# Performance work log

Measured on AMD Instinct MI355X. Metric: run time of the kernel, lower is better.

Reference implementation:

```python
import jax, jax.numpy as jnp
import numpy as np

H, NH, NL, FF, W, CMAX, V, L, G = 768, 12, 6, 3072, 256, 32, 50272, 4096, 64
DH = H // NH
SCALE = 1.0 / np.sqrt(DH)

def _ln(x, s, b, eps=1e-5):
    m = jnp.mean(x, -1, keepdims=True)
    v = jnp.mean((x - m) ** 2, -1, keepdims=True)
    return (x - m) * jax.lax.rsqrt(v + eps) * s + b

def _heads(x, B, Lx):
    return x.reshape(B, Lx, NH, DH).transpose(0, 2, 1, 3)  # [B,NH,L,DH]

def _layer(x, p, am, gpos, is_glob):
    (Wq, bq, Wk, bk, Wv, bv, Wqg, bqg, Wkg, bkg, Wvg, bvg, Wo, bo,
     ln1s, ln1b, W1, b1, W2, b2, ln2s, ln2b) = p
    B, Lx, _ = x.shape
    Nb = Lx // W
    q = _heads(x @ Wq + bq, B, Lx)
    k = _heads(x @ Wk + bk, B, Lx)
    v = _heads(x @ Wv + bv, B, Lx)
    qb = q.reshape(B, NH, Nb, W, DH)
    def ctx(t):  # gather 3 adjacent key/value blocks per query block
        tb = t.reshape(B, NH, Nb, W, DH)
        tp = jnp.pad(tb, ((0, 0), (0, 0), (1, 1), (0, 0), (0, 0)))
        return jnp.stack([tp[:, :, i:i + Nb] for i in range(3)], axis=3).reshape(B, NH, Nb, 3 * W, DH)
    k_ctx, v_ctx = ctx(k), ctx(v)
    s_loc = jnp.einsum('bhnqd,bhnkd->bhnqk', qb, k_ctx) * SCALE  # [B,NH,Nb,W,3W]
    rel = jnp.arange(3 * W)[None, :] - W - jnp.arange(W)[:, None]  # [W,3W]
    band = jnp.abs(rel) <= W
    pos = jnp.arange(Nb)[:, None] * W + jnp.arange(3 * W)[None, :] - W  # abs key pos [Nb,3W]
    inb = (pos >= 0) & (pos < Lx)
    safe = jnp.clip(pos, 0, Lx - 1)
    key_ok = inb & (~is_glob[safe]) & am[:, safe]  # [B,Nb,3W]; global keys handled separately
    mask = key_ok[:, None, :, None, :] & band[None, None, None, :, :]
    s_loc = jnp.where(mask, s_loc, -1e9)
    # every token also attends to the G global tokens (global K/V projections)
    kg = _heads(x @ Wkg + bkg, B, Lx)
    vg = _heads(x @ Wvg + bvg, B, Lx)
    kgs, vgs = kg[:, :, gpos], vg[:, :, gpos]  # [B,NH,G,DH]
    s_glb = jnp.einsum('bhnqd,bhgd->bhnqg', qb, kgs) * SCALE
    attn = jax.nn.softmax(jnp.concatenate([s_loc, s_glb], -1), axis=-1)
    a_loc, a_glb = attn[..., :3 * W], attn[..., 3 * W:]
    out = jnp.einsum('bhnqk,bhnkd->bhnqd', a_loc, v_ctx) + jnp.einsum('bhnqg,bhgd->bhnqd', a_glb, vgs)
    out = out.reshape(B, NH, Lx, DH)
    # global query rows: full attention over all positions, overwrite outputs
    qg = _heads(x @ Wqg + bqg, B, Lx)[:, :, gpos]  # [B,NH,G,DH]
    s_full = jnp.einsum('bhgd,bhld->bhgl', qg, kg) * SCALE
    s_full = jnp.where(am[:, None, None, :], s_full, -1e9)
    og = jnp.einsum('bhgl,bhld->bhgd', jax.nn.softmax(s_full, -1), vg)
    out = out.at[:, :, gpos].set(og)
    out = out.transpose(0, 2, 1, 3).reshape(B, Lx, H)
    x = _ln(x + out @ Wo + bo, ln1s, ln1b)
    h = jax.nn.gelu(x @ W1 + b1, approximate=False)
    x = _ln(x + h @ W2 + b2, ln2s, ln2b)
    return x

def _forward(floats, input_ids, attention_mask, global_positions, cand_token_id):
    (emb_tok, emb_pos, lnes, lneb,
     Wq, bq, Wk, bk, Wv, bv, Wqg, bqg, Wkg, bkg, Wvg, bvg, Wo, bo,
     ln1_s, ln1_b, W1, b1, W2, b2, ln2_s, ln2_b, Wh1, bh1, Wh2, bh2) = floats
    B, Lx = input_ids.shape
    x = _ln(emb_tok[input_ids] + emb_pos[None, :Lx], lnes, lneb)
    is_glob = jnp.zeros(Lx, bool).at[global_positions].set(True)
    layers = (Wq, bq, Wk, bk, Wv, bv, Wqg, bqg, Wkg, bkg, Wvg, bvg, Wo, bo,
              ln1_s, ln1_b, W1, b1, W2, b2, ln2_s, ln2_b)
    def step(xc, p):
        return _layer(xc, p, attention_mask, global_positions, is_glob), None
    x, _ = jax.lax.scan(step, x, layers)
    # ListwiseRankingHead: gather hidden states at [CAND] marker positions
    cand_mask = input_ids == cand_token_id
    order = jnp.argsort(jnp.where(cand_mask, 0, 1).astype(jnp.int32), axis=1)  # stable
    positions = order[:, :CMAX]
    valid = jnp.take_along_axis(cand_mask, positions, axis=1)
    g = jnp.take_along_axis(x, positions[..., None], axis=1)  # [B,CMAX,H]
    h = jax.nn.gelu(g @ Wh1 + bh1, approximate=False)  # dropout is eval no-op
    logits = (h @ Wh2 + bh2).squeeze(-1)
    return logits, valid

def setup_inputs() -> dict:
    key = jax.random.key(0)
    ks = iter(jax.random.split(key, 64))
    r = lambda shape: jax.random.normal(next(ks), shape, jnp.float32) * 0.02
    B, CAND = 1, 50265
    d = {
        'emb_tok': r((V, H)), 'emb_pos': r((L, H)),
        'ln_emb_s': jnp.ones((H,), jnp.float32), 'ln_emb_b': jnp.zeros((H,), jnp.float32),
        'Wq': r((NL, H, H)), 'bq': jnp.zeros((NL, H), jnp.float32),
        'Wk': r((NL, H, H)), 'bk': jnp.zeros((NL, H), jnp.float32),
        'Wv': r((NL, H, H)), 'bv': jnp.zeros((NL, H), jnp.float32),
        'Wqg': r((NL, H, H)), 'bqg': jnp.zeros((NL, H), jnp.float32),
        'Wkg': r((NL, H, H)), 'bkg': jnp.zeros((NL, H), jnp.float32),
        'Wvg': r((NL, H, H)), 'bvg': jnp.zeros((NL, H), jnp.float32),
        'Wo': r((NL, H, H)), 'bo': jnp.zeros((NL, H), jnp.float32),
        'ln1_s': jnp.ones((NL, H), jnp.float32), 'ln1_b': jnp.zeros((NL, H), jnp.float32),
        'W1': r((NL, H, FF)), 'b1': jnp.zeros((NL, FF), jnp.float32),
        'W2': r((NL, FF, H)), 'b2': jnp.zeros((NL, H), jnp.float32),
        'ln2_s': jnp.ones((NL, H), jnp.float32), 'ln2_b': jnp.zeros((NL, H), jnp.float32),
        'Wh1': r((H, H // 2)), 'bh1': jnp.zeros((H // 2,), jnp.float32),
        'Wh2': r((H // 2, 1)), 'bh2': jnp.zeros((1,), jnp.float32),
    }
    input_ids = jax.random.randint(next(ks), (B, L), 0, CAND, dtype=jnp.int32)
    cand_pos = 256 + 128 * jnp.arange(30)  # 30 [CAND] markers
    input_ids = input_ids.at[:, cand_pos].set(CAND)
    d['input_ids'] = input_ids
    d['attention_mask'] = jnp.ones((B, L), jnp.bool_)
    d['global_positions'] = jnp.concatenate([jnp.arange(34), cand_pos]).astype(jnp.int32)  # CLS+query+markers
    d['cand_token_id'] = CAND
    return d

def reference(emb_tok, emb_pos, ln_emb_s, ln_emb_b, Wq, bq, Wk, bk, Wv, bv,
              Wqg, bqg, Wkg, bkg, Wvg, bvg, Wo, bo, ln1_s, ln1_b,
              W1, b1, W2, b2, ln2_s, ln2_b, Wh1, bh1, Wh2, bh2,
              input_ids, attention_mask, global_positions, cand_token_id):
    floats = (emb_tok, emb_pos, ln_emb_s, ln_emb_b, Wq, bq, Wk, bk, Wv, bv,
              Wqg, bqg, Wkg, bkg, Wvg, bvg, Wo, bo, ln1_s, ln1_b,
              W1, b1, W2, b2, ln2_s, ln2_b, Wh1, bh1, Wh2, bh2)
    return _forward(floats, input_ids, attention_mask, global_positions, cand_token_id)
```

## Files before the change

### kernel.cpp

```cpp
#include <hip/hip_runtime.h>
#include <hip/hip_bf16.h>
#include <math.h>

#define H 768
#define NH 12
#define DH 64
#define NL 6
#define FF 3072
#define LL 4096
#define GG 64
#define NCMAX 32

#define MATSZ (H * H)
#define OFF_QG ((size_t)5 * MATSZ)
#define OFF_O  ((size_t)6 * MATSZ)
#define OFF_W1 ((size_t)7 * MATSZ)
#define OFF_W2 (OFF_W1 + (size_t)H * FF)
#define WT_ELEMS (OFF_W2 + (size_t)FF * H)

typedef unsigned short u16;
typedef __attribute__((ext_vector_type(8))) unsigned short us8;
typedef __attribute__((ext_vector_type(4))) unsigned short us4;
typedef __attribute__((ext_vector_type(8))) __bf16 bf16x8;
typedef __attribute__((ext_vector_type(4))) float f32x4;

__device__ __forceinline__ float bf2f(u16 u) {
  unsigned v = ((unsigned)u) << 16;
  return __builtin_bit_cast(float, v);
}
__device__ __forceinline__ u16 f2bf(float f) {
  unsigned u = __builtin_bit_cast(unsigned, f);
  unsigned r = (u + 0x7fffu + ((u >> 16) & 1u)) >> 16;
  return (u16)r;
}
__device__ __forceinline__ float geluf(float a) {
  return 0.5f * a * (1.f + erff(a * 0.70710678118654752440f));
}
__device__ __forceinline__ float wredsum(float v) {
  #pragma unroll
  for (int o = 32; o; o >>= 1) v += __shfl_xor(v, o);
  return v;
}
__device__ __forceinline__ float wredmax(float v) {
  #pragma unroll
  for (int o = 32; o; o >>= 1) v = fmaxf(v, __shfl_xor(v, o));
  return v;
}
__device__ __forceinline__ void gld16(const u16* g, u16* l) {
  __builtin_amdgcn_global_load_lds(
      (const __attribute__((address_space(1))) unsigned int*)(const void*)g,
      (__attribute__((address_space(3))) unsigned int*)(void*)l, 16, 0, 0);
}
__device__ __forceinline__ void tswz(int& bx, int& by) {
  int nx = gridDim.x, ny = gridDim.y;
  int flat = blockIdx.y * nx + blockIdx.x;
  int nwg = nx * ny;
  if ((nwg & 7) == 0) {
    int c = nwg >> 3;
    flat = (flat & 7) * c + (flat >> 3);
  }
  bx = flat % nx;
  by = flat / nx;
}

__global__ __launch_bounds__(256) void embed_ln_k(
    const float* __restrict__ et, const float* __restrict__ ep, const int* __restrict__ ids,
    const float* __restrict__ sc, const float* __restrict__ bi,
    float* __restrict__ x, u16* __restrict__ xb)
{
  int r = blockIdx.x, t = threadIdx.x;
  int tok = ids[r];
  if (tok < 0) tok = 0;
  if (tok >= 50272) tok = 50271;
  __shared__ float red[4];
  float v[3];
  #pragma unroll
  for (int e = 0; e < 3; ++e) {
    int c = t + e * 256;
    v[e] = et[(size_t)tok * H + c] + ep[(size_t)r * H + c];
  }
  float s = v[0] + v[1] + v[2];
  s = wredsum(s);
  if ((t & 63) == 0) red[t >> 6] = s;
  __syncthreads();
  float mean = (red[0] + red[1] + red[2] + red[3]) * (1.f / 768.f);
  __syncthreads();
  float q = 0.f;
  #pragma unroll
  for (int e = 0; e < 3; ++e) { float d = v[e] - mean; q += d * d; }
  q = wredsum(q);
  if ((t & 63) == 0) red[t >> 6] = q;
  __syncthreads();
  float var = (red[0] + red[1] + red[2] + red[3]) * (1.f / 768.f);
  float rs = rsqrtf(var + 1e-5f);
  #pragma unroll
  for (int e = 0; e < 3; ++e) {
    int c = t + e * 256;
    float o = (v[e] - mean) * rs * sc[c] + bi[c];
    x[(size_t)r * H + c] = o;
    xb[(size_t)r * H + c] = f2bf(o);
  }
}

__global__ __launch_bounds__(256) void ln_res_k(
    float* __restrict__ x, const float* __restrict__ bias,
    const float* __restrict__ sc, const float* __restrict__ bi, u16* __restrict__ xb)
{
  int r = blockIdx.x, t = threadIdx.x;
  __shared__ float red[4];
  float v[3];
  #pragma unroll
  for (int e = 0; e < 3; ++e) {
    int c = t + e * 256;
    v[e] = x[(size_t)r * H + c] + bias[c];
  }
  float s = v[0] + v[1] + v[2];
  s = wredsum(s);
  if ((t & 63) == 0) red[t >> 6] = s;
  __syncthreads();
  float mean = (red[0] + red[1] + red[2] + red[3]) * (1.f / 768.f);
  __syncthreads();
  float q = 0.f;
  #pragma unroll
  for (int e = 0; e < 3; ++e) { float d = v[e] - mean; q += d * d; }
  q = wredsum(q);
  if ((t & 63) == 0) red[t >> 6] = q;
  __syncthreads();
  float var = (red[0] + red[1] + red[2] + red[3]) * (1.f / 768.f);
  float rs = rsqrtf(var + 1e-5f);
  #pragma unroll
  for (int e = 0; e < 3; ++e) {
    int c = t + e * 256;
    float o = (v[e] - mean) * rs * sc[c] + bi[c];
    x[(size_t)r * H + c] = o;
    xb[(size_t)r * H + c] = f2bf(o);
  }
}

__global__ __launch_bounds__(256) void conv_layer_k(
    const float* __restrict__ Wq, const float* __restrict__ Wk, const float* __restrict__ Wv,
    const float* __restrict__ Wkg, const float* __restrict__ Wvg, const float* __restrict__ Wqg,
    const float* __restrict__ Wo, const float* __restrict__ W1, const float* __restrict__ W2,
    u16* __restrict__ wt)
{
  int bid = blockIdx.x, t = threadIdx.x;
  const float* src;
  size_t ooff;
  int K, N, tile;
  if (bid < 1008) {
    int m = bid / 144;
    tile = bid % 144;
    K = H; N = H;
    ooff = (size_t)m * MATSZ;
    src = m == 0 ? Wq : m == 1 ? Wk : m == 2 ? Wv : m == 3 ? Wkg : m == 4 ? Wvg : m == 5 ? Wqg : Wo;
  } else if (bid < 1584) {
    tile = bid - 1008;
    K = H; N = FF;
    ooff = OFF_W1;
    src = W1;
  } else {
    tile = bid - 1584;
    K = FF; N = H;
    ooff = OFF_W2;
    src = W2;
  }
  int KT = K / 64;
  int kt = tile % KT, nt = tile / KT;
  __shared__ u16 sT[64 * 72];
  #pragma unroll
  for (int it = 0; it < 16; ++it) {
    int idx = t + it * 256;
    int n = idx & 63, kk = idx >> 6;
    sT[n * 72 + kk] = f2bf(src[(size_t)(kt * 64 + kk) * N + nt * 64 + n]);
  }
  __syncthreads();
  #pragma unroll
  for (int it = 0; it < 2; ++it) {
    int idx = t + it * 256;
    int n = idx >> 3, k8 = idx & 7;
    us8 val = *reinterpret_cast<const us8*>(&sT[n * 72 + k8 * 8]);
    *reinterpret_cast<us8*>(&wt[ooff + (size_t)(nt * 64 + n) * K + kt * 64 + k8 * 8]) = val;
  }
}

template<bool GLD>
__device__ __forceinline__ void gemm_loop(
    const u16* __restrict__ A, const u16* __restrict__ Bt,
    int M, int N, int K, int m0, int n0, int kb, int ke,
    u16* lsA, u16* lsB, f32x4 acc[4][4])
{
  int t = threadIdx.x;
  int w = t >> 6, lane = t & 63;
  int cl = lane & 15, kgr = lane >> 4;
  int wm = (w >> 1) * 64, wn = (w & 1) * 64;
  us8 z8 = {0, 0, 0, 0, 0, 0, 0, 0};
  for (int k0 = kb; k0 < ke; k0 += 64) {
    if (GLD) {
      int ml = lane >> 3, k8 = lane & 7;
      #pragma unroll
      for (int it = 0; it < 4; ++it) {
        int chunk = it * 4 + w;
        int m = chunk * 8 + ml;
        gld16(A + (size_t)(m0 + m) * K + k0 + ((k8 ^ (m & 7)) * 8),
              &lsA[chunk * 512 + lane * 8]);
      }
      #pragma unroll
      for (int it = 0; it < 4; ++it) {
        int chunk = it * 4 + w;
        int n = chunk * 8 + ml;
        gld16(Bt + (size_t)(n0 + n) * K + k0 + ((k8 ^ (n & 7)) * 8),
              &lsB[chunk * 512 + lane * 8]);
      }
    } else {
      #pragma unroll
      for (int it = 0; it < 4; ++it) {
        int c = t + it * 256;
        int m = c >> 3, k8 = c & 7;
        us8 val = z8;
        int gm = m0 + m;
        if (gm < M) val = *reinterpret_cast<const us8*>(A + (size_t)gm * K + k0 + k8 * 8);
        *reinterpret_cast<us8*>(&lsA[m * 64 + ((k8 ^ (m & 7)) * 8)]) = val;
      }
      #pragma unroll
      for (int it = 0; it < 4; ++it) {
        int c = t + it * 256;
        int n = c >> 3, k8 = c & 7;
        us8 val = *reinterpret_cast<const us8*>(Bt + (size_t)(n0 + n) * K + k0 + k8 * 8);
        *reinterpret_cast<us8*>(&lsB[n * 64 + ((k8 ^ (n & 7)) * 8)]) = val;
      }
    }
    __syncthreads();
    #pragma unroll
    for (int kk = 0; kk < 2; ++kk) {
      bf16x8 fa[4], fb[4];
      int k8 = kk * 4 + kgr;
      #pragma unroll
      for (int i = 0; i < 4; ++i) {
        int mr = wm + i * 16 + cl;
        fa[i] = __builtin_bit_cast(bf16x8,
            *reinterpret_cast<const us8*>(&lsA[mr * 64 + ((k8 ^ (mr & 7)) * 8)]));
        int nr = wn + i * 16 + cl;
        fb[i] = __builtin_bit_cast(bf16x8,
            *reinterpret_cast<const us8*>(&lsB[nr * 64 + ((k8 ^ (nr & 7)) * 8)]));
      }
      #pragma unroll
      for (int i = 0; i < 4; ++i)
        #pragma unroll
        for (int j = 0; j < 4; ++j)
          acc[i][j] = __builtin_amdgcn_mfma_f32_16x16x32_bf16(fa[i], fb[j], acc[i][j], 0, 0, 0);
    }
    __syncthreads();
  }
}

template<int ACT, bool GLD>
__global__ __launch_bounds__(256) void gemm_bias_k(
    const u16* __restrict__ A, const u16* __restrict__ Bt, const float* __restrict__ bias,
    u16* __restrict__ outB, int M, int N, int K)
{
  __shared__ u16 lsA[128 * 64];
  __shared__ u16 lsB[128 * 64];
  int bx, by;
  tswz(bx, by);
  int m0 = by * 128, n0 = bx * 128;
  f32x4 zero4 = {0.f, 0.f, 0.f, 0.f};
  f32x4 acc[4][4];
  #pragma unroll
  for (int i = 0; i < 4; ++i)
    #pragma unroll
    for (int j = 0; j < 4; ++j) acc[i][j] = zero4;
  gemm_loop<GLD>(A, Bt, M, N, K, m0, n0, 0, K, lsA, lsB, acc);
  int lane = threadIdx.x & 63, w = threadIdx.x >> 6;
  int cl = lane & 15, kgr = lane >> 4;
  int wm = (w >> 1) * 64, wn = (w & 1) * 64;
  #pragma unroll
  for (int j = 0; j < 4; ++j) {
    int n = n0 + wn + j * 16 + cl;
    float bv = bias[n];
    #pragma unroll
    for (int i = 0; i < 4; ++i) {
      #pragma unroll
      for (int r = 0; r < 4; ++r) {
        int m = m0 + wm + i * 16 + kgr * 4 + r;
        if (m < M) {
          float vv = acc[i][j][r] + bv;
          if (ACT == 1) vv = geluf(vv);
          outB[(size_t)m * N + n] = f2bf(vv);
        }
      }
    }
  }
}

__global__ __launch_bounds__(256) void gemm_acc_k(
    const u16* __restrict__ A, const u16* __restrict__ Bt, float* __restrict__ outF,
    int M, int N, int K)
{
  __shared__ u16 lsA[128 * 64];
  __shared__ u16 lsB[128 * 64];
  int bx, by;
  tswz(bx, by);
  int m0 = by * 128, n0 = bx * 128;
  int z = blockIdx.z, ns = gridDim.z;
  int ks = K / ns;
  f32x4 zero4 = {0.f, 0.f, 0.f, 0.f};
  f32x4 acc[4][4];
  #pragma unroll
  for (int i = 0; i < 4; ++i)
    #pragma unroll
    for (int j = 0; j < 4; ++j) acc[i][j] = zero4;
  gemm_loop<true>(A, Bt, M, N, K, m0, n0, z * ks, (z + 1) * ks, lsA, lsB, acc);
  int lane = threadIdx.x & 63, w = threadIdx.x >> 6;
  int cl = lane & 15, kgr = lane >> 4;
  int wm = (w >> 1) * 64, wn = (w & 1) * 64;
  #pragma unroll
  for (int j = 0; j < 4; ++j) {
    int n = n0 + wn + j * 16 + cl;
    #pragma unroll
    for (int i = 0; i < 4; ++i) {
      #pragma unroll
      for (int r = 0; r < 4; ++r) {
        int m = m0 + wm + i * 16 + kgr * 4 + r;
        atomicAdd(&outF[(size_t)m * N + n], acc[i][j][r]);
      }
    }
  }
}

__global__ __launch_bounds__(256) void gemm_qkv_k(
    const u16* __restrict__ A, const u16* __restrict__ wt,
    const float* c0, const float* c1, const float* c2, const float* c3, const float* c4,
    u16* o0, u16* o1, u16* o2, u16* o3, u16* o4)
{
  __shared__ u16 lsA[128 * 64];
  __shared__ u16 lsB[128 * 64];
  int z = blockIdx.z;
  const u16* Bt = wt + (size_t)z * MATSZ;
  const float* bias = z == 0 ? c0 : z == 1 ? c1 : z == 2 ? c2 : z == 3 ? c3 : c4;
  u16* outB = z == 0 ? o0 : z == 1 ? o1 : z == 2 ? o2 : z == 3 ? o3 : o4;
  int bx, by;
  tswz(bx, by);
  int m0 = by * 128, n0 = bx * 128;
  f32x4 zero4 = {0.f, 0.f, 0.f, 0.f};
  f32x4 acc[4][4];
  #pragma unroll
  for (int i = 0; i < 4; ++i)
    #pragma unroll
    for (int j = 0; j < 4; ++j) acc[i][j] = zero4;
  gemm_loop<true>(A, Bt, LL, H, H, m0, n0, 0, H, lsA, lsB, acc);
  int lane = threadIdx.x & 63, w = threadIdx.x >> 6;
  int cl = lane & 15, kgr = lane >> 4;
  int wm = (w >> 1) * 64, wn = (w & 1) * 64;
  #pragma unroll
  for (int j = 0; j < 4; ++j) {
    int n = n0 + wn + j * 16 + cl;
    float bv = bias[n];
    #pragma unroll
    for (int i = 0; i < 4; ++i) {
      #pragma unroll
      for (int r = 0; r < 4; ++r) {
        int m = m0 + wm + i * 16 + kgr * 4 + r;
        outB[(size_t)m * H + n] = f2bf(acc[i][j][r] + bv);
      }
    }
  }
}

__global__ __launch_bounds__(256) void attn_local_k(
    const u16* __restrict__ q, const u16* __restrict__ k, const u16* __restrict__ v,
    const u16* __restrict__ kgp, const u16* __restrict__ vgp,
    const int* __restrict__ gpos, const unsigned char* __restrict__ isg,
    u16* __restrict__ out)
{
  int h = blockIdx.x;
  int q0 = blockIdx.y * 64;
  int nb = q0 >> 8;
  int cs = (nb - 1) * 256;
  int cstart = (q0 >> 6) & 3;
  int t = threadIdx.x;
  int w = t >> 6, lane = t & 63;
  int cl = lane & 15, g = lane >> 4;
  __shared__ u16 sK[64 * 64];
  __shared__ u16 sVt[64 * 64];
  __shared__ u16 sP[64 * 64];
  __shared__ unsigned char sOk[64];
  us8 z8 = {0, 0, 0, 0, 0, 0, 0, 0};
  f32x4 zero4 = {0.f, 0.f, 0.f, 0.f};

  int qrow = q0 + w * 16 + cl;
  bf16x8 qa[2];
  #pragma unroll
  for (int ks = 0; ks < 2; ++ks)
    qa[ks] = __builtin_bit_cast(bf16x8, *reinterpret_cast<const us8*>(
        &q[(size_t)qrow * H + h * 64 + ks * 32 + g * 8]));

  f32x4 O[4];
  #pragma unroll
  for (int dt = 0; dt < 4; ++dt) O[dt] = zero4;
  float mrow[4], lrow[4];
  #pragma unroll
  for (int r = 0; r < 4; ++r) { mrow[r] = -1e30f; lrow[r] = 0.f; }

  for (int ci = 0; ci < 10; ++ci) {
    bool isLocal = (ci < 9);
    int kbase = cs + (cstart + ci) * 64;
    #pragma unroll
    for (int it = 0; it < 2; ++it) {
      int idx = t + it * 256;
      int key = idx >> 3, d8 = idx & 7;
      us8 val = z8;
      if (isLocal) {
        int pos = kbase + key;
        if (pos >= 0 && pos < LL)
          val = *reinterpret_cast<const us8*>(&k[(size_t)pos * H + h * 64 + d8 * 8]);
      } else {
        int pos = gpos[key];
        if (pos < 0) pos = 0;
        if (pos >= LL) pos = LL - 1;
        val = *reinterpret_cast<const us8*>(&kgp[(size_t)pos * H + h * 64 + d8 * 8]);
      }
      *reinterpret_cast<us8*>(&sK[key * 64 + ((d8 ^ (key & 7)) * 8)]) = val;
    }
    #pragma unroll
    for (int it = 0; it < 2; ++it) {
      int idx = t + it * 256;
      int key = idx >> 3, d8 = idx & 7;
      us8 val = z8;
      if (isLocal) {
        int pos = kbase + key;
        if (pos >= 0 && pos < LL)
          val = *reinterpret_cast<const us8*>(&v[(size_t)pos * H + h * 64 + d8 * 8]);
      } else {
        int pos = gpos[key];
        if (pos < 0) pos = 0;
        if (pos >= LL) pos = LL - 1;
        val = *reinterpret_cast<const us8*>(&vgp[(size_t)pos * H + h * 64 + d8 * 8]);
      }
      int k8 = key >> 3, klow = key & 7;
      int kswz = (k8 ^ d8) * 8 + klow;
      #pragma unroll
      for (int u = 0; u < 8; ++u)
        sVt[(d8 * 8 + u) * 64 + kswz] = val[u];
    }
    if (t < 64) {
      int ok = 1;
      if (isLocal) {
        int pos = kbase + t;
        ok = (pos >= 0 && pos < LL) ? (isg[pos] ? 0 : 1) : 0;
      }
      sOk[t] = (unsigned char)ok;
    }
    __syncthreads();

    f32x4 S[4];
    #pragma unroll
    for (int T = 0; T < 4; ++T) {
      S[T] = zero4;
      int key = T * 16 + cl;
      #pragma unroll
      for (int ks = 0; ks < 2; ++ks) {
        bf16x8 kf = __builtin_bit_cast(bf16x8, *reinterpret_cast<const us8*>(
            &sK[key * 64 + (((ks * 4 + g) ^ (key & 7)) * 8)]));
        S[T] = __builtin_amdgcn_mfma_f32_16x16x32_bf16(qa[ks], kf, S[T], 0, 0, 0);
      }
    }
    #pragma unroll
    for (int T = 0; T < 4; ++T) {
      int key = T * 16 + cl;
      int okk = sOk[key];
      int pos = kbase + key;
      #pragma unroll
      for (int r = 0; r < 4; ++r) {
        int qp = q0 + w * 16 + g * 4 + r;
        int d = pos - qp;
        bool ok = okk && (!isLocal || (d >= -256 && d <= 256));
        S[T][r] = ok ? S[T][r] * 0.125f : -1e9f;
      }
    }
    float cm[4];
    #pragma unroll
    for (int r = 0; r < 4; ++r) {
      cm[r] = fmaxf(fmaxf(S[0][r], S[1][r]), fmaxf(S[2][r], S[3][r]));
      cm[r] = fmaxf(cm[r], __shfl_xor(cm[r], 1));
      cm[r] = fmaxf(cm[r], __shfl_xor(cm[r], 2));
      cm[r] = fmaxf(cm[r], __shfl_xor(cm[r], 4));
      cm[r] = fmaxf(cm[r], __shfl_xor(cm[r], 8));
    }
    float sc[4];
    #pragma unroll
    for (int r = 0; r < 4; ++r) {
      float mn = fmaxf(mrow[r], cm[r]);
      sc[r] = __expf(mrow[r] - mn);
      mrow[r] = mn;
    }
    float rs[4] = {0.f, 0.f, 0.f, 0.f};
    #pragma unroll
    for (int T = 0; T < 4; ++T) {
      int key = T * 16 + cl;
      #pragma unroll
      for (int r = 0; r < 4; ++r) {
        float sv = S[T][r];
        float pv = sv > -1e8f ? __expf(sv - mrow[r]) : 0.f;
        rs[r] += pv;
        int qloc = w * 16 + g * 4 + r;
        int k8s = (key >> 3) ^ (qloc & 7);
        sP[qloc * 64 + k8s * 8 + (key & 7)] = f2bf(pv);
      }
    }
    #pragma unroll
    for (int r = 0; r < 4; ++r) {
      rs[r] += __shfl_xor(rs[r], 1);
      rs[r] += __shfl_xor(rs[r], 2);
      rs[r] += __shfl_xor(rs[r], 4);
      rs[r] += __shfl_xor(rs[r], 8);
      lrow[r] = lrow[r] * sc[r] + rs[r];
    }
    #pragma unroll
    for (int dt = 0; dt < 4; ++dt)
      #pragma unroll
      for (int r = 0; r < 4; ++r) O[dt][r] *= sc[r];
    int prow = w * 16 + cl;
    #pragma unroll
    for (int ks = 0; ks < 2; ++ks) {
      bf16x8 pf = __builtin_bit_cast(bf16x8, *reinterpret_cast<const us8*>(
          &sP[prow * 64 + (((ks * 4 + g) ^ (prow & 7)) * 8)]));
      #pragma unroll
      for (int dt = 0; dt < 4; ++dt) {
        int dim = dt * 16 + cl;
        int k8s = (ks * 4 + g) ^ ((dim >> 3) & 7);
        bf16x8 vf = __builtin_bit_cast(bf16x8, *reinterpret_cast<const us8*>(
            &sVt[dim * 64 + k8s * 8]));
        O[dt] = __builtin_amdgcn_mfma_f32_16x16x32_bf16(pf, vf, O[dt], 0, 0, 0);
      }
    }
    __syncthreads();
  }
  #pragma unroll
  for (int r = 0; r < 4; ++r) {
    float inv = 1.f / lrow[r];
    int qp = q0 + w * 16 + g * 4 + r;
    #pragma unroll
    for (int dt = 0; dt < 4; ++dt)
      out[(size_t)qp * H + h * 64 + dt * 16 + cl] = f2bf(O[dt][r] * inv);
  }
}

__global__ __launch_bounds__(256) void ag_score_k(
    const u16* __restrict__ qg, const u16* __restrict__ kg, float* __restrict__ sbuf)
{
  int h = blockIdx.x;
  int kc0 = blockIdx.y * 128;
  int t = threadIdx.x;
  int w = t >> 6, lane = t & 63;
  int cl = lane & 15, g = lane >> 4;
  __shared__ u16 sK[128 * 64];
  #pragma unroll
  for (int it = 0; it < 4; ++it) {
    int c = t + it * 256;
    int key = c >> 3, d8 = c & 7;
    us8 val = *reinterpret_cast<const us8*>(&kg[(size_t)(kc0 + key) * H + h * 64 + d8 * 8]);
    *reinterpret_cast<us8*>(&sK[key * 64 + ((d8 ^ (key & 7)) * 8)]) = val;
  }
  int qrow = w * 16 + cl;
  bf16x8 qa[2];
  #pragma unroll
  for (int ks = 0; ks < 2; ++ks)
    qa[ks] = __builtin_bit_cast(bf16x8, *reinterpret_cast<const us8*>(
        &qg[(size_t)qrow * H + h * 64 + ks * 32 + g * 8]));
  __syncthreads();
  f32x4 zero4 = {0.f, 0.f, 0.f, 0.f};
  #pragma unroll
  for (int j = 0; j < 8; ++j) {
    f32x4 S = zero4;
    int key = j * 16 + cl;
    #pragma unroll
    for (int ks = 0; ks < 2; ++ks) {
      bf16x8 kf = __builtin_bit_cast(bf16x8, *reinterpret_cast<const us8*>(
          &sK[key * 64 + (((ks * 4 + g) ^ (key & 7)) * 8)]));
      S = __builtin_amdgcn_mfma_f32_16x16x32_bf16(qa[ks], kf, S, 0, 0, 0);
    }
    #pragma unroll
    for (int r = 0; r < 4; ++r) {
      int grow = w * 16 + g * 4 + r;
      sbuf[((size_t)(h * 64 + grow)) * 4096 + kc0 + key] = S[r] * 0.125f;
    }
  }
}

__global__ __launch_bounds__(256) void ag_soft_k(float* __restrict__ sbuf)
{
  int row = blockIdx.x, t = threadIdx.x;
  float* base = sbuf + (size_t)row * 4096;
  u16* pb = (u16*)(sbuf) + (size_t)row * 8192;
  __shared__ float red[4];
  f32x4 rv[4];
  #pragma unroll
  for (int it = 0; it < 4; ++it)
    rv[it] = *reinterpret_cast<const f32x4*>(base + it * 1024 + t * 4);
  float m = -1e30f;
  #pragma unroll
  for (int it = 0; it < 4; ++it)
    #pragma unroll
    for (int u = 0; u < 4; ++u) m = fmaxf(m, rv[it][u]);
  m = wredmax(m);
  if ((t & 63) == 0) red[t >> 6] = m;
  __syncthreads();
  m = fmaxf(fmaxf(red[0], red[1]), fmaxf(red[2], red[3]));
  __syncthreads();
  float s = 0.f;
  #pragma unroll
  for (int it = 0; it < 4; ++it)
    #pragma unroll
    for (int u = 0; u < 4; ++u) {
      float e = __expf(rv[it][u] - m);
      rv[it][u] = e;
      s += e;
    }
  s = wredsum(s);
  if ((t & 63) == 0) red[t >> 6] = s;
  __syncthreads();
  float inv = 1.f / (red[0] + red[1] + red[2] + red[3]);
  #pragma unroll
  for (int it = 0; it < 4; ++it) {
    us4 o;
    #pragma unroll
    for (int u = 0; u < 4; ++u) o[u] = f2bf(rv[it][u] * inv);
    *reinterpret_cast<us4*>(pb + it * 1024 + t * 4) = o;
  }
}

__global__ __launch_bounds__(256) void ag_pv_k(
    const float* __restrict__ sbuf, const u16* __restrict__ vg, float* __restrict__ obuf)
{
  int h = blockIdx.x;
  int kb0 = blockIdx.y * 256;
  int t = threadIdx.x;
  int w = t >> 6, lane = t & 63;
  int cl = lane & 15, g = lane >> 4;
  __shared__ u16 sVt[64 * 64];
  f32x4 zero4 = {0.f, 0.f, 0.f, 0.f};
  f32x4 O[4];
  #pragma unroll
  for (int dt = 0; dt < 4; ++dt) O[dt] = zero4;
  const u16* pb = (const u16*)(sbuf);
  int prow = w * 16 + cl;
  size_t pbase = (size_t)(h * 64 + prow) * 8192;

  for (int cc = 0; cc < 4; ++cc) {
    int kc = kb0 + cc * 64;
    #pragma unroll
    for (int it = 0; it < 2; ++it) {
      int idx = t + it * 256;
      int key = idx >> 3, d8 = idx & 7;
      us8 val = *reinterpret_cast<const us8*>(&vg[(size_t)(kc + key) * H + h * 64 + d8 * 8]);
      int k8 = key >> 3, klow = key & 7;
      int kswz = (k8 ^ d8) * 8 + klow;
      #pragma unroll
      for (int u = 0; u < 8; ++u)
        sVt[(d8 * 8 + u) * 64 + kswz] = val[u];
    }
    __syncthreads();
    #pragma unroll
    for (int ks = 0; ks < 2; ++ks) {
      bf16x8 pf = __builtin_bit_cast(bf16x8, *reinterpret_cast<const us8*>(
          pb + pbase + kc + (ks * 4 + g) * 8));
      #pragma unroll
      for (int dt = 0; dt < 4; ++dt) {
        int dim = dt * 16 + cl;
        int k8s = (ks * 4 + g) ^ ((dim >> 3) & 7);
        bf16x8 vf = __builtin_bit_cast(bf16x8, *reinterpret_cast<const us8*>(
            &sVt[dim * 64 + k8s * 8]));
        O[dt] = __builtin_amdgcn_mfma_f32_16x16x32_bf16(pf, vf, O[dt], 0, 0, 0);
      }
    }
    __syncthreads();
  }
  #pragma unroll
  for (int r = 0; r < 4; ++r) {
    int grow = w * 16 + g * 4 + r;
    #pragma unroll
    for (int dt = 0; dt < 4; ++dt)
      atomicAdd(&obuf[((size_t)h * 64 + grow) * 64 + dt * 16 + cl], O[dt][r]);
  }
}

__global__ __launch_bounds__(256) void ag_write_k(
    float* __restrict__ obuf, const int* __restrict__ gpos, u16* __restrict__ out)
{
  int g = blockIdx.x, t = threadIdx.x;
  int gp = gpos[g];
  if (gp < 0) gp = 0;
  if (gp >= LL) gp = LL - 1;
  #pragma unroll
  for (int e = 0; e < 3; ++e) {
    int c = t + e * 256;
    int h = c >> 6, d = c & 63;
    size_t idx = ((size_t)h * 64 + g) * 64 + d;
    out[(size_t)gp * H + c] = f2bf(obuf[idx]);
    obuf[idx] = 0.f;
  }
}

__global__ void isglob_k(const int* __restrict__ gpos, unsigned char* __restrict__ isg) {
  int t = threadIdx.x;
  for (int i = t; i < LL; i += 256) isg[i] = 0;
  __syncthreads();
  if (t < GG) {
    int gp = gpos[t];
    if (gp >= 0 && gp < LL) isg[gp] = 1;
  }
}

__global__ void gather_k(const u16* __restrict__ xb, const int* __restrict__ gpos,
                         u16* __restrict__ xgb) {
  int g = blockIdx.x, t = threadIdx.x;
  int p = gpos[g];
  if (p < 0) p = 0;
  if (p >= LL) p = LL - 1;
  #pragma unroll
  for (int e = 0; e < 3; ++e)
    xgb[(size_t)g * H + t + e * 256] = xb[(size_t)p * H + t + e * 256];
}

__global__ void positions_k(const int* __restrict__ ids, const int* __restrict__ candp,
                            int* __restrict__ posb, float* __restrict__ outp) {
  int t = threadIdx.x;
  int cand = candp[0];
  __shared__ int cnt[257];
  int base = t * 16, c0 = 0;
  for (int u = 0; u < 16; ++u) c0 += (ids[base + u] == cand) ? 1 : 0;
  cnt[t + 1] = c0;
  __syncthreads();
  if (t == 0) {
    cnt[0] = 0;
    for (int i2 = 1; i2 <= 256; ++i2) cnt[i2] += cnt[i2 - 1];
  }
  __syncthreads();
  int ncand = cnt[256];
  int cr = cnt[t];
  for (int u = 0; u < 16; ++u) {
    int i2 = base + u;
    bool isC = (ids[i2] == cand);
    if (isC) {
      if (cr < NCMAX) posb[cr] = i2;
      cr++;
    } else {
      int nc = i2 - cr;
      int slot = ncand + nc;
      if (slot < NCMAX && nc >= 0) posb[slot] = i2;
    }
  }
  if (t < NCMAX) outp[NCMAX + t] = (t < ncand) ? 1.f : 0.f;
}

__global__ __launch_bounds__(256) void head_k(
    const float* __restrict__ x, const int* __restrict__ posb,
    const float* __restrict__ Wh1, const float* __restrict__ bh1,
    const float* __restrict__ Wh2, const float* __restrict__ bh2, float* __restrict__ outp) {
  int s = blockIdx.x, t = threadIdx.x;
  int p = posb[s];
  if (p < 0) p = 0;
  if (p >= LL) p = LL - 1;
  __shared__ float sx[H];
  __shared__ float sh[384];
  __shared__ float red[4];
  #pragma unroll
  for (int e = 0; e < 3; ++e) sx[t + e * 256] = x[(size_t)p * H + t + e * 256];
  __syncthreads();
  for (int j = t; j < 384; j += 256) {
    float a = bh1[j];
    for (int c = 0; c < H; ++c) a += sx[c] * Wh1[(size_t)c * 384 + j];
    sh[j] = geluf(a);
  }
  __syncthreads();
  float part = 0.f;
  for (int j = t; j < 384; j += 256) part += sh[j] * Wh2[j];
  part = wredsum(part);
  if ((t & 63) == 0) red[t >> 6] = part;
  __syncthreads();
  if (t == 0) {
    float tot = red[0] + red[1] + red[2] + red[3] + bh2[0];
    outp[s] = tot;
  }
}

extern "C" void kernel_launch(void* const* d_in, const int* in_sizes, int n_in,
                              void* d_out, int out_size, void* d_ws, size_t ws_size,
                              hipStream_t stream) {
  const float* emb_tok = (const float*)d_in[0];
  const float* emb_pos = (const float*)d_in[1];
  const float* lnes = (const float*)d_in[2];
  const float* lneb = (const float*)d_in[3];
  const float* Wq = (const float*)d_in[4];
  const float* bq = (const float*)d_in[5];
  const float* Wk = (const float*)d_in[6];
  const float* bk = (const float*)d_in[7];
  const float* Wv = (const float*)d_in[8];
  const float* bv = (const float*)d_in[9];
  const float* Wqg = (const float*)d_in[10];
  const float* bqg = (const float*)d_in[11];
  const float* Wkg = (const float*)d_in[12];
  const float* bkg = (const float*)d_in[13];
  const float* Wvg = (const float*)d_in[14];
  const float* bvg = (const float*)d_in[15];
  const float* Wo = (const float*)d_in[16];
  const float* bo = (const float*)d_in[17];
  const float* ln1s = (const float*)d_in[18];
  const float* ln1b = (const float*)d_in[19];
  const float* W1 = (const float*)d_in[20];
  const float* b1 = (const float*)d_in[21];
  const float* W2 = (const float*)d_in[22];
  const float* b2 = (const float*)d_in[23];
  const float* ln2s = (const float*)d_in[24];
  const float* ln2b = (const float*)d_in[25];
  const float* Wh1 = (const float*)d_in[26];
  const float* bh1 = (const float*)d_in[27];
  const float* Wh2 = (const float*)d_in[28];
  const float* bh2 = (const float*)d_in[29];
  const int* ids = (const int*)d_in[30];
  int i_gpos = 32, i_cand = 33;
  if (!(n_in >= 34 && in_sizes[32] == GG)) {
    if (n_in >= 33 && in_sizes[31] == GG) { i_gpos = 31; i_cand = 32; }
  }
  const int* gpos = (const int*)d_in[i_gpos];
  const int* cand = (const int*)d_in[i_cand];
  float* outp = (float*)d_out;

  char* p = (char*)d_ws;
  auto alloc = [&](size_t bytes) {
    char* r = p;
    p += (bytes + 255) & ~(size_t)255;
    return r;
  };
  float* x = (float*)alloc((size_t)LL * H * 4);
  u16* xb = (u16*)alloc((size_t)LL * H * 2);
  u16* qb = (u16*)alloc((size_t)LL * H * 2);
  u16* kb = (u16*)alloc((size_t)LL * H * 2);
  u16* vb = (u16*)alloc((size_t)LL * H * 2);
  u16* kgb = (u16*)alloc((size_t)LL * H * 2);
  u16* vgb = (u16*)alloc((size_t)LL * H * 2);
  u16* ob = (u16*)alloc((size_t)LL * H * 2);
  u16* qgb = (u16*)alloc((size_t)GG * H * 2);
  u16* xgb = (u16*)alloc((size_t)GG * H * 2);
  unsigned char* isg = (unsigned char*)alloc(LL);
  int* posb = (int*)alloc(64 * 4);
  u16* wtb = (u16*)alloc(WT_ELEMS * 2);
  float* sbuf = (float*)alloc((size_t)NH * 64 * 4096 * 4);
  float* obuf = (float*)alloc((size_t)NH * 64 * 64 * 4);
  u16* hb = qb;

  hipMemsetAsync(obuf, 0, (size_t)NH * 64 * 64 * 4, stream);

  embed_ln_k<<<LL, 256, 0, stream>>>(emb_tok, emb_pos, ids, lnes, lneb, x, xb);
  isglob_k<<<1, 256, 0, stream>>>(gpos, isg);
  positions_k<<<1, 256, 0, stream>>>(ids, cand, posb, outp);

  dim3 gP2(H / 128, LL / 128, 2);
  dim3 gP4(H / 128, LL / 128, 4);
  dim3 gF(FF / 128, LL / 128);
  dim3 gQKV(H / 128, LL / 128, 5);
  for (int l = 0; l < NL; ++l) {
    size_t lo = (size_t)l * H * H;
    conv_layer_k<<<2160, 256, 0, stream>>>(
        Wq + lo, Wk + lo, Wv + lo, Wkg + lo, Wvg + lo, Wqg + lo, Wo + lo,
        W1 + (size_t)l * H * FF, W2 + (size_t)l * FF * H, wtb);
    gemm_qkv_k<<<gQKV, 256, 0, stream>>>(xb, wtb,
        bq + l * H, bk + l * H, bv + l * H, bkg + l * H, bvg + l * H,
        qb, kb, vb, kgb, vgb);
    gather_k<<<GG, 256, 0, stream>>>(xb, gpos, xgb);
    gemm_bias_k<0, true><<<dim3(H / 128, 1), 256, 0, stream>>>(
        xgb, wtb + OFF_QG, bqg + l * H, qgb, GG, H, H);
    attn_local_k<<<dim3(NH, LL / 64), 256, 0, stream>>>(qb, kb, vb, kgb, vgb, gpos, isg, ob);
    ag_score_k<<<dim3(NH, LL / 128), 256, 0, stream>>>(qgb, kgb, sbuf);
    ag_soft_k<<<NH * 64, 256, 0, stream>>>(sbuf);
    ag_pv_k<<<dim3(NH, LL / 256), 256, 0, stream>>>(sbuf, vgb, obuf);
    ag_write_k<<<GG, 256, 0, stream>>>(obuf, gpos, ob);
    gemm_acc_k<<<gP2, 256, 0, stream>>>(ob, wtb + OFF_O, x, LL, H, H);
    ln_res_k<<<LL, 256, 0, stream>>>(x, bo + l * H, ln1s + l * H, ln1b + l * H, xb);
    gemm_bias_k<1, true><<<gF, 256, 0, stream>>>(
        xb, wtb + OFF_W1, b1 + l * FF, hb, LL, FF, H);
    gemm_acc_k<<<gP4, 256, 0, stream>>>(hb, wtb + OFF_W2, x, LL, H, FF);
    ln_res_k<<<LL, 256, 0, stream>>>(x, b2 + l * H, ln2s + l * H, ln2b + l * H, xb);
  }
  head_k<<<NCMAX, 256, 0, stream>>>(x, posb, Wh1, bh1, Wh2, bh2, outp);
}
```

Baseline: 1.653 ms.

## Batch weight conversion, fuse global-query GEMM into QKV, replace split-K atomics with partials

Weight conversion to bf16 now runs once for all six layers in a single launch instead of once per layer. The global-query projection becomes a sixth z-slice of the QKV GEMM, so a separate launch goes away. The split-K output and FFN GEMMs write per-slice partial buffers that the LayerNorm kernel sums, replacing fp32 atomicAdd on the residual. The attention K-tile loads switch to direct global-to-LDS loads. In exchange it uses more workspace (all layers' weights plus four full-size fp32 partial buffers) and adds extra partial-buffer reads in LayerNorm.

```diff
diff --git a/kernel.cpp b/kernel.cpp
--- a/kernel.cpp
+++ b/kernel.cpp
@@ -102,8 +102,9 @@
   }
 }
 
-__global__ __launch_bounds__(256) void ln_res_k(
-    float* __restrict__ x, const float* __restrict__ bias,
+template<int Z>
+__global__ __launch_bounds__(256) void ln_res2_k(
+    float* __restrict__ x, const float* __restrict__ part, const float* __restrict__ bias,
     const float* __restrict__ sc, const float* __restrict__ bi, u16* __restrict__ xb)
 {
   int r = blockIdx.x, t = threadIdx.x;
@@ -112,7 +113,11 @@
   #pragma unroll
   for (int e = 0; e < 3; ++e) {
     int c = t + e * 256;
-    v[e] = x[(size_t)r * H + c] + bias[c];
+    float a = x[(size_t)r * H + c] + bias[c];
+    #pragma unroll
+    for (int z = 0; z < Z; ++z)
+      a += part[(size_t)z * LL * H + (size_t)r * H + c];
+    v[e] = a;
   }
   float s = v[0] + v[1] + v[2];
   s = wredsum(s);
@@ -137,13 +142,17 @@
   }
 }
 
-__global__ __launch_bounds__(256) void conv_layer_k(
+__global__ __launch_bounds__(256) void conv_all_k(
     const float* __restrict__ Wq, const float* __restrict__ Wk, const float* __restrict__ Wv,
     const float* __restrict__ Wkg, const float* __restrict__ Wvg, const float* __restrict__ Wqg,
     const float* __restrict__ Wo, const float* __restrict__ W1, const float* __restrict__ W2,
     u16* __restrict__ wt)
 {
+  int l = blockIdx.y;
   int bid = blockIdx.x, t = threadIdx.x;
+  size_t lo = (size_t)l * MATSZ;
+  size_t lf = (size_t)l * H * FF;
+  u16* wto = wt + (size_t)l * WT_ELEMS;
   const float* src;
   size_t ooff;
   int K, N, tile;
@@ -152,17 +161,17 @@
     tile = bid % 144;
     K = H; N = H;
     ooff = (size_t)m * MATSZ;
-    src = m == 0 ? Wq : m == 1 ? Wk : m == 2 ? Wv : m == 3 ? Wkg : m == 4 ? Wvg : m == 5 ? Wqg : Wo;
+    src = (m == 0 ? Wq : m == 1 ? Wk : m == 2 ? Wv : m == 3 ? Wkg : m == 4 ? Wvg : m == 5 ? Wqg : Wo) + lo;
   } else if (bid < 1584) {
     tile = bid - 1008;
     K = H; N = FF;
     ooff = OFF_W1;
-    src = W1;
+    src = W1 + lf;
   } else {
     tile = bid - 1584;
     K = FF; N = H;
     ooff = OFF_W2;
-    src = W2;
+    src = W2 + lf;
   }
   int KT = K / 64;
   int kt = tile % KT, nt = tile / KT;
@@ -179,69 +188,48 @@
     int idx = t + it * 256;
     int n = idx >> 3, k8 = idx & 7;
     us8 val = *reinterpret_cast<const us8*>(&sT[n * 72 + k8 * 8]);
-    *reinterpret_cast<us8*>(&wt[ooff + (size_t)(nt * 64 + n) * K + kt * 64 + k8 * 8]) = val;
-  }
-}
-
-template<bool GLD>
+    *reinterpret_cast<us8*>(&wto[ooff + (size_t)(nt * 64 + n) * K + kt * 64 + k8 * 8]) = val;
+  }
+}
+
 __device__ __forceinline__ void gemm_loop(
     const u16* __restrict__ A, const u16* __restrict__ Bt,
-    int M, int N, int K, int m0, int n0, int kb, int ke,
+    int K, int m0, int n0, int kb, int ke,
     u16* lsA, u16* lsB, f32x4 acc[4][4])
 {
   int t = threadIdx.x;
   int w = t >> 6, lane = t & 63;
   int cl = lane & 15, kgr = lane >> 4;
   int wm = (w >> 1) * 64, wn = (w & 1) * 64;
-  us8 z8 = {0, 0, 0, 0, 0, 0, 0, 0};
   for (int k0 = kb; k0 < ke; k0 += 64) {
-    if (GLD) {
-      int ml = lane >> 3, k8 = lane & 7;
-      #pragma unroll
-      for (int it = 0; it < 4; ++it) {
-        int chunk = it * 4 + w;
-        int m = chunk * 8 + ml;
-        gld16(A + (size_t)(m0 + m) * K + k0 + ((k8 ^ (m & 7)) * 8),
-              &lsA[chunk * 512 + lane * 8]);
-      }
-      #pragma unroll
-      for (int it = 0; it < 4; ++it) {
-        int chunk = it * 4 + w;
-        int n = chunk * 8 + ml;
-        gld16(Bt + (size_t)(n0 + n) * K + k0 + ((k8 ^ (n & 7)) * 8),
-              &lsB[chunk * 512 + lane * 8]);
-      }
-    } else {
-      #pragma unroll
-      for (int it = 0; it < 4; ++it) {
-        int c = t + it * 256;
-        int m = c >> 3, k8 = c & 7;
-        us8 val = z8;
-        int gm = m0 + m;
-        if (gm < M) val = *reinterpret_cast<const us8*>(A + (size_t)gm * K + k0 + k8 * 8);
-        *reinterpret_cast<us8*>(&lsA[m * 64 + ((k8 ^ (m & 7)) * 8)]) = val;
-      }
-      #pragma unroll
-      for (int it = 0; it < 4; ++it) {
-        int c = t + it * 256;
-        int n = c >> 3, k8 = c & 7;
-        us8 val = *reinterpret_cast<const us8*>(Bt + (size_t)(n0 + n) * K + k0 + k8 * 8);
-        *reinterpret_cast<us8*>(&lsB[n * 64 + ((k8 ^ (n & 7)) * 8)]) = val;
-      }
+    int ml = lane >> 3, k8 = lane & 7;
+    #pragma unroll
+    for (int it = 0; it < 4; ++it) {
+      int chunk = it * 4 + w;
+      int m = chunk * 8 + ml;
+      gld16(A + (size_t)(m0 + m) * K + k0 + ((k8 ^ (m & 7)) * 8),
+            &lsA[chunk * 512 + lane * 8]);
+    }
+    #pragma unroll
+    for (int it = 0; it < 4; ++it) {
+      int chunk = it * 4 + w;
+      int n = chunk * 8 + ml;
+      gld16(Bt + (size_t)(n0 + n) * K + k0 + ((k8 ^ (n & 7)) * 8),
+            &lsB[chunk * 512 + lane * 8]);
     }
     __syncthreads();
     #pragma unroll
     for (int kk = 0; kk < 2; ++kk) {
       bf16x8 fa[4], fb[4];
-      int k8 = kk * 4 + kgr;
+      int k8r = kk * 4 + kgr;
       #pragma unroll
       for (int i = 0; i < 4; ++i) {
         int mr = wm + i * 16 + cl;
         fa[i] = __builtin_bit_cast(bf16x8,
-            *reinterpret_cast<const us8*>(&lsA[mr * 64 + ((k8 ^ (mr & 7)) * 8)]));
+            *reinterpret_cast<const us8*>(&lsA[mr * 64 + ((k8r ^ (mr & 7)) * 8)]));
         int nr = wn + i * 16 + cl;
         fb[i] = __builtin_bit_cast(bf16x8,
-            *reinterpret_cast<const us8*>(&lsB[nr * 64 + ((k8 ^ (nr & 7)) * 8)]));
+            *reinterpret_cast<const us8*>(&lsB[nr * 64 + ((k8r ^ (nr & 7)) * 8)]));
       }
       #pragma unroll
       for (int i = 0; i < 4; ++i)
@@ -253,7 +241,7 @@
   }
 }
 
-template<int ACT, bool GLD>
+template<int ACT>
 __global__ __launch_bounds__(256) void gemm_bias_k(
     const u16* __restrict__ A, const u16* __restrict__ Bt, const float* __restrict__ bias,
     u16* __restrict__ outB, int M, int N, int K)
@@ -269,7 +257,7 @@
   for (int i = 0; i < 4; ++i)
     #pragma unroll
     for (int j = 0; j < 4; ++j) acc[i][j] = zero4;
-  gemm_loop<GLD>(A, Bt, M, N, K, m0, n0, 0, K, lsA, lsB, acc);
+  gemm_loop(A, Bt, K, m0, n0, 0, K, lsA, lsB, acc);
   int lane = threadIdx.x & 63, w = threadIdx.x >> 6;
   int cl = lane & 15, kgr = lane >> 4;
   int wm = (w >> 1) * 64, wn = (w & 1) * 64;
@@ -292,8 +280,8 @@
   }
 }
 
-__global__ __launch_bounds__(256) void gemm_acc_k(
-    const u16* __restrict__ A, const u16* __restrict__ Bt, float* __restrict__ outF,
+__global__ __launch_bounds__(256) void gemm_part_k(
+    const u16* __restrict__ A, const u16* __restrict__ Bt, float* __restrict__ part,
     int M, int N, int K)
 {
   __shared__ u16 lsA[128 * 64];
@@ -309,10 +297,11 @@
   for (int i = 0; i < 4; ++i)
     #pragma unroll
     for (int j = 0; j < 4; ++j) acc[i][j] = zero4;
-  gemm_loop<true>(A, Bt, M, N, K, m0, n0, z * ks, (z + 1) * ks, lsA, lsB, acc);
+  gemm_loop(A, Bt, K, m0, n0, z * ks, (z + 1) * ks, lsA, lsB, acc);
   int lane = threadIdx.x & 63, w = threadIdx.x >> 6;
   int cl = lane & 15, kgr = lane >> 4;
   int wm = (w >> 1) * 64, wn = (w & 1) * 64;
+  float* po = part + (size_t)z * LL * H;
   #pragma unroll
   for (int j = 0; j < 4; ++j) {
     int n = n0 + wn + j * 16 + cl;
@@ -321,25 +310,29 @@
       #pragma unroll
       for (int r = 0; r < 4; ++r) {
         int m = m0 + wm + i * 16 + kgr * 4 + r;
-        atomicAdd(&outF[(size_t)m * N + n], acc[i][j][r]);
+        po[(size_t)m * N + n] = acc[i][j][r];
       }
     }
   }
 }
 
 __global__ __launch_bounds__(256) void gemm_qkv_k(
-    const u16* __restrict__ A, const u16* __restrict__ wt,
+    const u16* __restrict__ A, const u16* __restrict__ Ag, const u16* __restrict__ wt,
     const float* c0, const float* c1, const float* c2, const float* c3, const float* c4,
-    u16* o0, u16* o1, u16* o2, u16* o3, u16* o4)
+    const float* c5,
+    u16* o0, u16* o1, u16* o2, u16* o3, u16* o4, u16* o5)
 {
   __shared__ u16 lsA[128 * 64];
   __shared__ u16 lsB[128 * 64];
   int z = blockIdx.z;
-  const u16* Bt = wt + (size_t)z * MATSZ;
-  const float* bias = z == 0 ? c0 : z == 1 ? c1 : z == 2 ? c2 : z == 3 ? c3 : c4;
-  u16* outB = z == 0 ? o0 : z == 1 ? o1 : z == 2 ? o2 : z == 3 ? o3 : o4;
   int bx, by;
   tswz(bx, by);
+  if (z == 5 && by != 0) return;
+  const u16* Bt = wt + (size_t)z * MATSZ;
+  const float* bias = z == 0 ? c0 : z == 1 ? c1 : z == 2 ? c2 : z == 3 ? c3 : z == 4 ? c4 : c5;
+  u16* outB = z == 0 ? o0 : z == 1 ? o1 : z == 2 ? o2 : z == 3 ? o3 : z == 4 ? o4 : o5;
+  const u16* Ap = (z == 5) ? Ag : A;
+  int M = (z == 5) ? GG : LL;
   int m0 = by * 128, n0 = bx * 128;
   f32x4 zero4 = {0.f, 0.f, 0.f, 0.f};
   f32x4 acc[4][4];
@@ -347,7 +340,7 @@
   for (int i = 0; i < 4; ++i)
     #pragma unroll
     for (int j = 0; j < 4; ++j) acc[i][j] = zero4;
-  gemm_loop<true>(A, Bt, LL, H, H, m0, n0, 0, H, lsA, lsB, acc);
+  gemm_loop(Ap, Bt, H, m0, n0, 0, H, lsA, lsB, acc);
   int lane = threadIdx.x & 63, w = threadIdx.x >> 6;
   int cl = lane & 15, kgr = lane >> 4;
   int wm = (w >> 1) * 64, wn = (w & 1) * 64;
@@ -360,7 +353,7 @@
       #pragma unroll
       for (int r = 0; r < 4; ++r) {
         int m = m0 + wm + i * 16 + kgr * 4 + r;
-        outB[(size_t)m * H + n] = f2bf(acc[i][j][r] + bv);
+        if (m < M) outB[(size_t)m * H + n] = f2bf(acc[i][j][r] + bv);
       }
     }
   }
@@ -406,20 +399,18 @@
     int kbase = cs + (cstart + ci) * 64;
     #pragma unroll
     for (int it = 0; it < 2; ++it) {
-      int idx = t + it * 256;
+      int idx = it * 256 + t;
       int key = idx >> 3, d8 = idx & 7;
-      us8 val = z8;
+      int pos;
       if (isLocal) {
-        int pos = kbase + key;
-        if (pos >= 0 && pos < LL)
-          val = *reinterpret_cast<const us8*>(&k[(size_t)pos * H + h * 64 + d8 * 8]);
+        pos = kbase + key;
+        pos = pos < 0 ? 0 : (pos >= LL ? LL - 1 : pos);
       } else {
-        int pos = gpos[key];
-        if (pos < 0) pos = 0;
-        if (pos >= LL) pos = LL - 1;
-        val = *reinterpret_cast<const us8*>(&kgp[(size_t)pos * H + h * 64 + d8 * 8]);
-      }
-      *reinterpret_cast<us8*>(&sK[key * 64 + ((d8 ^ (key & 7)) * 8)]) = val;
+        pos = gpos[key];
+        pos = pos < 0 ? 0 : (pos >= LL ? LL - 1 : pos);
+      }
+      const u16* src = (isLocal ? k : kgp) + (size_t)pos * H + h * 64 + ((d8 ^ (key & 7)) * 8);
+      gld16(src, &sK[idx * 8]);
     }
     #pragma unroll
     for (int it = 0; it < 2; ++it) {
@@ -556,10 +547,9 @@
   __shared__ u16 sK[128 * 64];
   #pragma unroll
   for (int it = 0; it < 4; ++it) {
-    int c = t + it * 256;
-    int key = c >> 3, d8 = c & 7;
-    us8 val = *reinterpret_cast<const us8*>(&kg[(size_t)(kc0 + key) * H + h * 64 + d8 * 8]);
-    *reinterpret_cast<us8*>(&sK[key * 64 + ((d8 ^ (key & 7)) * 8)]) = val;
+    int idx = it * 256 + t;
+    int key = idx >> 3, d8 = idx & 7;
+    gld16(kg + (size_t)(kc0 + key) * H + h * 64 + ((d8 ^ (key & 7)) * 8), &sK[idx * 8]);
   }
   int qrow = w * 16 + cl;
   bf16x8 qa[2];
@@ -841,16 +831,18 @@
   u16* vgb = (u16*)alloc((size_t)LL * H * 2);
   u16* ob = (u16*)alloc((size_t)LL * H * 2);
   u16* qgb = (u16*)alloc((size_t)GG * H * 2);
-  u16* xgb = (u16*)alloc((size_t)GG * H * 2);
+  u16* xgb = (u16*)alloc((size_t)128 * H * 2);
   unsigned char* isg = (unsigned char*)alloc(LL);
   int* posb = (int*)alloc(64 * 4);
-  u16* wtb = (u16*)alloc(WT_ELEMS * 2);
+  u16* wtb = (u16*)alloc((size_t)NL * WT_ELEMS * 2);
   float* sbuf = (float*)alloc((size_t)NH * 64 * 4096 * 4);
   float* obuf = (float*)alloc((size_t)NH * 64 * 64 * 4);
+  float* partb = (float*)alloc((size_t)4 * LL * H * 4);
   u16* hb = qb;
 
   hipMemsetAsync(obuf, 0, (size_t)NH * 64 * 64 * 4, stream);
 
+  conv_all_k<<<dim3(2160, NL), 256, 0, stream>>>(Wq, Wk, Wv, Wkg, Wvg, Wqg, Wo, W1, W2, wtb);
   embed_ln_k<<<LL, 256, 0, stream>>>(emb_tok, emb_pos, ids, lnes, lneb, x, xb);
   isglob_k<<<1, 256, 0, stream>>>(gpos, isg);
   positions_k<<<1, 256, 0, stream>>>(ids, cand, posb, outp);
@@ -858,29 +850,23 @@
   dim3 gP2(H / 128, LL / 128, 2);
   dim3 gP4(H / 128, LL / 128, 4);
   dim3 gF(FF / 128, LL / 128);
-  dim3 gQKV(H / 128, LL / 128, 5);
+  dim3 gQKV(H / 128, LL / 128, 6);
   for (int l = 0; l < NL; ++l) {
-    size_t lo = (size_t)l * H * H;
-    conv_layer_k<<<2160, 256, 0, stream>>>(
-        Wq + lo, Wk + lo, Wv + lo, Wkg + lo, Wvg + lo, Wqg + lo, Wo + lo,
-        W1 + (size_t)l * H * FF, W2 + (size_t)l * FF * H, wtb);
-    gemm_qkv_k<<<gQKV, 256, 0, stream>>>(xb, wtb,
-        bq + l * H, bk + l * H, bv + l * H, bkg + l * H, bvg + l * H,
-        qb, kb, vb, kgb, vgb);
+    u16* wt = wtb + (size_t)l * WT_ELEMS;
     gather_k<<<GG, 256, 0, stream>>>(xb, gpos, xgb);
-    gemm_bias_k<0, true><<<dim3(H / 128, 1), 256, 0, stream>>>(
-        xgb, wtb + OFF_QG, bqg + l * H, qgb, GG, H, H);
+    gemm_qkv_k<<<gQKV, 256, 0, stream>>>(xb, xgb, wt,
+        bq + l * H, bk + l * H, bv + l * H, bkg + l * H, bvg + l * H, bqg + l * H,
+        qb, kb, vb, kgb, vgb, qgb);
     attn_local_k<<<dim3(NH, LL / 64), 256, 0, stream>>>(qb, kb, vb, kgb, vgb, gpos, isg, ob);
     ag_score_k<<<dim3(NH, LL / 128), 256, 0, stream>>>(qgb, kgb, sbuf);
     ag_soft_k<<<NH * 64, 256, 0, stream>>>(sbuf);
     ag_pv_k<<<dim3(NH, LL / 256), 256, 0, stream>>>(sbuf, vgb, obuf);
     ag_write_k<<<GG, 256, 0, stream>>>(obuf, gpos, ob);
-    gemm_acc_k<<<gP2, 256, 0, stream>>>(ob, wtb + OFF_O, x, LL, H, H);
-    ln_res_k<<<LL, 256, 0, stream>>>(x, bo + l * H, ln1s + l * H, ln1b + l * H, xb);
-    gemm_bias_k<1, true><<<gF, 256, 0, stream>>>(
-        xb, wtb + OFF_W1, b1 + l * FF, hb, LL, FF, H);
-    gemm_acc_k<<<gP4, 256, 0, stream>>>(hb, wtb + OFF_W2, x, LL, H, FF);
-    ln_res_k<<<LL, 256, 0, stream>>>(x, b2 + l * H, ln2s + l * H, ln2b + l * H, xb);
+    gemm_part_k<<<gP2, 256, 0, stream>>>(ob, wt + OFF_O, partb, LL, H, H);
+    ln_res2_k<2><<<LL, 256, 0, stream>>>(x, partb, bo + l * H, ln1s + l * H, ln1b + l * H, xb);
+    gemm_bias_k<1><<<gF, 256, 0, stream>>>(xb, wt + OFF_W1, b1 + l * FF, hb, LL, FF, H);
+    gemm_part_k<<<gP4, 256, 0, stream>>>(hb, wt + OFF_W2, partb, LL, H, FF);
+    ln_res2_k<4><<<LL, 256, 0, stream>>>(x, partb, b2 + l * H, ln2s + l * H, ln2b + l * H, xb);
   }
   head_k<<<NCMAX, 256, 0, stream>>>(x, posb, Wh1, bh1, Wh2, bh2, outp);
 }
```

After: 1.460 ms. -11.7%, faster.
